# Performance work log

Measured on AMD Instinct MI355X. Metric: run time of the kernel, lower is better.

## Reference

```python
import jax, jax.numpy as jnp
import numpy as np

N_TRANSFORMS = 24
N_INIT = 5
SOFT_BLEND = 5.0
MAX_STEPS = 8   # reduced from 50 for reference runtime; same per-step math
CVG = 1e-5
DVG = 1.0
EPS = 1e-6


def posi_enc(x):
    # min_deg=0, max_deg=4, append_identity: [...,3] -> [...,27]
    scales = jnp.asarray([1.0, 2.0, 4.0, 8.0], x.dtype)
    xb = (x[..., None, :] * scales[:, None]).reshape(x.shape[:-1] + (12,))
    return jnp.concatenate([x, jnp.sin(xb), jnp.cos(xb)], axis=-1)


def mlp(h, params):
    for W, b in params[:-1]:
        h = jax.nn.relu(h @ W + b)
    W, b = params[-1]
    return h @ W + b


def setup_inputs() -> dict:
    key = jax.random.key(0)
    ks = jax.random.split(key, 16)
    B, N, J = 1, 32768, N_TRANSFORMS
    x = jax.random.normal(ks[0], (B, N, 3), jnp.float32)
    bone_pts = jax.random.normal(ks[1], (J, 3), jnp.float32)

    def near_id(k):
        A = jnp.eye(4, dtype=jnp.float32) + 0.05 * jax.random.normal(k, (J, 4, 4), jnp.float32)
        return A.at[:, 3, :].set(jnp.asarray([0.0, 0.0, 0.0, 1.0], jnp.float32))

    inp = dict(
        x=x, bone_pts=bone_pts,
        transforms=near_id(ks[2]), delta_transforms=near_id(ks[3]),
        W0=0.1 * jax.random.normal(ks[4], (27, 128), jnp.float32), b0=jnp.zeros((128,), jnp.float32),
        W1=0.1 * jax.random.normal(ks[5], (128, 128), jnp.float32), b1=jnp.zeros((128,), jnp.float32),
        W2=0.1 * jax.random.normal(ks[6], (128, 128), jnp.float32), b2=jnp.zeros((128,), jnp.float32),
        W3=0.1 * jax.random.normal(ks[7], (128, 128), jnp.float32), b3=jnp.zeros((128,), jnp.float32),
        W4=0.1 * jax.random.normal(ks[8], (128, 25), jnp.float32), b4=jnp.zeros((25,), jnp.float32),
    )
    return inp


def reference(x, bone_pts, transforms, delta_transforms, W0, b0, W1, b1, W2, b2, W3, b3, W4, b4):
    params = [(W0, b0), (W1, b1), (W2, b2), (W3, b3), (W4, b4)]
    B, N, _ = x.shape
    I = N_INIT + 1  # with_bkgd appends identity init
    dt = x.dtype

    # ---- _initialize_canonical: KNN over bone distances, gather delta transforms
    d = jnp.linalg.norm(x[:, :, None, :] - bone_pts, axis=-1)          # [B,N,J]
    idx = jax.lax.top_k(-d, N_INIT)[1]                                  # [B,N,5]
    Tsel = delta_transforms[idx]                                        # [B,N,5,4,4]
    eye4 = jnp.broadcast_to(jnp.eye(4, dtype=dt), (B, N, 1, 4, 4))
    Tinit = jnp.concatenate([Tsel, eye4], axis=2)                       # [B,N,I,4,4]
    xh = jnp.concatenate([x, jnp.ones_like(x[..., :1])], axis=-1)
    xc0 = jnp.einsum('bnipq,bnq->bnip', Tinit[..., :3, :4], xh)         # [B,N,I,3]

    M = B * N * I
    target = jnp.broadcast_to(x[:, :, None, :], (B, N, I, 3)).reshape(M, 3)
    x0 = xc0.reshape(M, 3)
    Tfull = jnp.concatenate([transforms, jnp.eye(4, dtype=dt)[None]], axis=0)  # [J+1,4,4]

    def g(xc):  # forward-skinning residual g(x_cano) = LBS(x_cano) - x_world
        w = jax.nn.softmax(SOFT_BLEND * mlp(posi_enc(xc), params), axis=-1)   # [M,25]
        tf = jnp.einsum('mj,jpq->mpq', w, Tfull)                               # [M,4,4]
        return jnp.einsum('mpq,mq->mp', tf[:, :3, :3], xc) + tf[:, :3, 3] - target

    # ---- Broyden with dense per-point masking (replaces torch boolean indexing)
    Jinv0 = jnp.broadcast_to(jnp.eye(3, dtype=dt), (M, 3, 3))
    gx0 = g(x0)
    upd0 = -(Jinv0 @ gx0[:, :, None])[:, :, 0]
    norm0 = jnp.linalg.norm(gx0, axis=-1)
    zeros3 = jnp.zeros((M, 3), dt)
    state = (x0, gx0, Jinv0, upd0, x0, norm0, zeros3, zeros3, jnp.ones((M,), bool))

    def body(_, s):
        xk, gx, Jinv, upd, xopt, nopt, dx, dgx, mask = s
        m3 = mask[:, None]
        dx = jnp.where(m3, upd, dx)
        xk = jnp.where(m3, xk + dx, xk)
        gnew = g(xk)
        dgx = jnp.where(m3, gnew - gx, dgx)
        gx = jnp.where(m3, gx + dgx, gx)
        gn = jnp.linalg.norm(gx, axis=-1)
        better = gn < nopt
        nopt = jnp.where(better, gn, nopt)
        xopt = jnp.where(better[:, None], xk, xopt)
        mask = (nopt > CVG) & (gn < DVG)
        vT = dx[:, None, :] @ Jinv                                      # [M,1,3]
        a = dx[:, :, None] - Jinv @ dgx[:, :, None]                      # [M,3,1]
        b = vT @ dgx[:, :, None]                                         # [M,1,1]
        b = b + jnp.where(b >= 0, EPS, -EPS)
        Jinv = jnp.where(mask[:, None, None], Jinv + (a / b) @ vT, Jinv)
        upd = jnp.where(m3, -(Jinv @ gx[:, :, None])[:, :, 0], upd)
        return (xk, gx, Jinv, upd, xopt, nopt, dx, dgx, mask)

    state = jax.lax.fori_loop(0, MAX_STEPS, body, state)
    xopt, nopt = state[4], state[5]
    xopt = jax.lax.stop_gradient(xopt)  # torch detaches the root solve
    valid = nopt < CVG

    # differentiable final forward skinning at the found canonical points
    w = jax.nn.softmax(SOFT_BLEND * mlp(posi_enc(xopt), params), axis=-1)
    tf = jnp.einsum('mj,jpq->mpq', w, Tfull)
    xw = jnp.einsum('mpq,mq->mp', tf[:, :3, :3], xopt) + tf[:, :3, 3]

    return (xw.reshape(B, N, I, 3), xopt.reshape(B, N, I, 3),
            nopt.reshape(B, N, I), valid.reshape(B, N, I))
```

## Files before the change

### kernel.cpp

```cpp
#include <hip/hip_runtime.h>
#include <math.h>
#include <stdint.h>

#define BLOCK 64
#define PPW 32
#define NTILES 56

typedef float v2f __attribute__((ext_vector_type(2)));

__device__ __forceinline__ v2f mkv2(float a, float b) {
    v2f r; r.x = a; r.y = b; return r;
}
__device__ __forceinline__ v2f pkfma(v2f a, v2f b, v2f c) {
#if __has_builtin(__builtin_elementwise_fma)
    return __builtin_elementwise_fma(a, b, c);
#else
    return mkv2(fmaf(a.x, b.x, c.x), fmaf(a.y, b.y, c.y));
#endif
}
__device__ __forceinline__ float f4el(const float4& v, int r) {
    return (r == 0) ? v.x : (r == 1) ? v.y : (r == 2) ? v.z : v.w;
}

#define VMWAIT() asm volatile("s_waitcnt vmcnt(0)" ::: "memory")

__device__ __forceinline__ void stage_tile(const float* __restrict__ Wt, int t,
                                           float* dst, int lane) {
    const float* src = Wt + t * 1024 + lane * 4;
    float* d0 = dst + lane * 4;
    __builtin_amdgcn_global_load_lds(
        (const __attribute__((address_space(1))) uint32_t*)src,
        (__attribute__((address_space(3))) uint32_t*)d0, 16, 0, 0);
    __builtin_amdgcn_global_load_lds(
        (const __attribute__((address_space(1))) uint32_t*)(src + 256),
        (__attribute__((address_space(3))) uint32_t*)(d0 + 256), 16, 0, 0);
    __builtin_amdgcn_global_load_lds(
        (const __attribute__((address_space(1))) uint32_t*)(src + 512),
        (__attribute__((address_space(3))) uint32_t*)(d0 + 512), 16, 0, 0);
    __builtin_amdgcn_global_load_lds(
        (const __attribute__((address_space(1))) uint32_t*)(src + 768),
        (__attribute__((address_space(3))) uint32_t*)(d0 + 768), 16, 0, 0);
}

__global__ void prep_kernel(const float* __restrict__ W0, const float* __restrict__ W1,
                            const float* __restrict__ W2, const float* __restrict__ W3,
                            const float* __restrict__ W4, const float* __restrict__ b4,
                            float* __restrict__ Wt, float* __restrict__ b4p) {
    const int d = blockIdx.x * blockDim.x + threadIdx.x;
    if (d < NTILES * 1024) {
        const int t = d >> 10, w = d & 1023;
        float v;
        if (t < 52) {
            const int r = w >> 7, rem = w & 127;
            const int half = rem >> 6, q = (rem >> 2) & 15, jl = rem & 3;
            const int col = q * 8 + half * 4 + jl;
            if (t < 4)       { const int k = t * 8 + r;        v = (k < 27) ? W0[k * 128 + col] : 0.f; }
            else if (t < 20) { const int k = (t - 4) * 8 + r;  v = W1[k * 128 + col]; }
            else if (t < 36) { const int k = (t - 20) * 8 + r; v = W2[k * 128 + col]; }
            else             { const int k = (t - 36) * 8 + r; v = W3[k * 128 + col]; }
        } else {
            const int r = w >> 5, c = w & 31;
            const int k = (t - 52) * 32 + r;
            v = (c < 25) ? W4[k * 25 + c] : 0.f;
        }
        Wt[d] = v;
    }
    if (d < 32) b4p[d] = (d < 25) ? b4[d] : 0.f;
}

__device__ __forceinline__ void batch2(const float* wt, int kt, int cg,
                                       const float* hgg, int kh,
                                       v2f* __restrict__ acc) {
    const float4 w00 = *(const float4*)(wt + kt * 128 + cg * 4);
    const float4 w01 = *(const float4*)(wt + kt * 128 + 64 + cg * 4);
    const float4 w10 = *(const float4*)(wt + (kt + 1) * 128 + cg * 4);
    const float4 w11 = *(const float4*)(wt + (kt + 1) * 128 + 64 + cg * 4);
    v2f h[8];
#pragma unroll
    for (int j = 0; j < 8; ++j) h[j] = *(const v2f*)(hgg + j * 132 + kh);
    const v2f a0 = mkv2(w00.x, w00.y), a1 = mkv2(w00.z, w00.w);
    const v2f a2 = mkv2(w01.x, w01.y), a3 = mkv2(w01.z, w01.w);
    const v2f b0v = mkv2(w10.x, w10.y), b1v = mkv2(w10.z, w10.w);
    const v2f b2v = mkv2(w11.x, w11.y), b3v = mkv2(w11.z, w11.w);
#pragma unroll
    for (int j = 0; j < 8; ++j) {
        v2f hh = mkv2(h[j].x, h[j].x);
        acc[j * 4 + 0] = pkfma(hh, a0, acc[j * 4 + 0]);
        acc[j * 4 + 1] = pkfma(hh, a1, acc[j * 4 + 1]);
        acc[j * 4 + 2] = pkfma(hh, a2, acc[j * 4 + 2]);
        acc[j * 4 + 3] = pkfma(hh, a3, acc[j * 4 + 3]);
        hh = mkv2(h[j].y, h[j].y);
        acc[j * 4 + 0] = pkfma(hh, b0v, acc[j * 4 + 0]);
        acc[j * 4 + 1] = pkfma(hh, b1v, acc[j * 4 + 1]);
        acc[j * 4 + 2] = pkfma(hh, b2v, acc[j * 4 + 2]);
        acc[j * 4 + 3] = pkfma(hh, b3v, acc[j * 4 + 3]);
    }
}

template <int NT>
__device__ __forceinline__ void main_layer(const float* __restrict__ Wt,
                                           const float* __restrict__ bL,
                                           float (*wb)[1024], int& cur, int& gt,
                                           const float* hgg, float* hwr,
                                           int cg, int lane) {
    v2f acc[32];
    {
        const float4 bb0 = *(const float4*)(bL + 8 * cg);
        const float4 bb1 = *(const float4*)(bL + 8 * cg + 4);
#pragma unroll
        for (int j = 0; j < 8; ++j) {
            acc[j * 4 + 0] = mkv2(bb0.x, bb0.y);
            acc[j * 4 + 1] = mkv2(bb0.z, bb0.w);
            acc[j * 4 + 2] = mkv2(bb1.x, bb1.y);
            acc[j * 4 + 3] = mkv2(bb1.z, bb1.w);
        }
    }
#pragma unroll 1
    for (int t = 0; t < NT; ++t) {
        VMWAIT();
        stage_tile(Wt, (gt == 55) ? 0 : (gt + 1), &wb[cur ^ 1][0], lane);
        const float* wt = &wb[cur][0];
#pragma unroll
        for (int b = 0; b < 4; ++b)
            batch2(wt, b * 2, cg, hgg, t * 8 + b * 2, acc);
        cur ^= 1;
        ++gt;
    }
#pragma unroll
    for (int j = 0; j < 8; ++j) {
        float4 o0, o1;
        o0.x = fmaxf(acc[j * 4 + 0].x, 0.f); o0.y = fmaxf(acc[j * 4 + 0].y, 0.f);
        o0.z = fmaxf(acc[j * 4 + 1].x, 0.f); o0.w = fmaxf(acc[j * 4 + 1].y, 0.f);
        o1.x = fmaxf(acc[j * 4 + 2].x, 0.f); o1.y = fmaxf(acc[j * 4 + 2].y, 0.f);
        o1.z = fmaxf(acc[j * 4 + 3].x, 0.f); o1.w = fmaxf(acc[j * 4 + 3].y, 0.f);
        *(float4*)(hwr + j * 132) = o0;
        *(float4*)(hwr + j * 132 + 4) = o1;
    }
}

__global__ __launch_bounds__(BLOCK)
__attribute__((amdgpu_num_vgpr(128))) void snarf_kernel(
    const float* __restrict__ xin, const float* __restrict__ bone_pts,
    const float* __restrict__ transforms, const float* __restrict__ delta_tf,
    const float* __restrict__ Wt, const float* __restrict__ b0,
    const float* __restrict__ b1, const float* __restrict__ b2,
    const float* __restrict__ b3, const float* __restrict__ b4p,
    float* __restrict__ out, int Npts) {
    __shared__ float hL[4248];
    __shared__ float stL[25 * PPW];
    __shared__ float wb[2][1024];
    const int lane = threadIdx.x;
    const int cg = lane >> 2;
    const int gg = lane & 3;
    const int p32 = lane & 31;
    const int du = lane >> 5;
    const int M = Npts * 6;
    const int m = blockIdx.x * PPW + p32;
    const int mc = (m < M) ? m : (M - 1);
    const int n = mc / 6;
    const int i = mc - n * 6;

    float* hq = hL + p32 * 132 + ((p32 >> 3) << 3);
    const float* hgg = hL + gg * 1064;
    float* hwr = hL + gg * 1064 + 8 * cg;
    volatile float* st = &stL[p32];
#define STS(idx) st[(idx) * PPW]

    stage_tile(Wt, 0, &wb[0][0], lane);
    int cur = 0;

    const float tx = xin[n * 3 + 0], ty = xin[n * 3 + 1], tz = xin[n * 3 + 2];

    float xk0, xk1, xk2;
    if (i < 5) {
        float dprev = -1.0f;
        int jprev = -1;
        for (int r = 0; r <= i; ++r) {
            float bd = 3.4028235e38f;
            int bj = 0;
            for (int j = 0; j < 24; ++j) {
                const float ax = tx - bone_pts[j * 3 + 0];
                const float ay = ty - bone_pts[j * 3 + 1];
                const float az = tz - bone_pts[j * 3 + 2];
                const float d = sqrtf(ax * ax + ay * ay + az * az);
                const bool taken = (d < dprev) || (d == dprev && j <= jprev);
                if (!taken && d < bd) { bd = d; bj = j; }
            }
            dprev = bd;
            jprev = bj;
        }
        const float* T = delta_tf + jprev * 16;
        xk0 = fmaf(T[0], tx, fmaf(T[1], ty, fmaf(T[2], tz, T[3])));
        xk1 = fmaf(T[4], tx, fmaf(T[5], ty, fmaf(T[6], tz, T[7])));
        xk2 = fmaf(T[8], tx, fmaf(T[9], ty, fmaf(T[10], tz, T[11])));
    } else {
        xk0 = tx; xk1 = ty; xk2 = tz;
    }

    float gx0 = 0.f, gx1 = 0.f, gx2 = 0.f;
    bool mask = (m < M);

    for (int step = -1; step < 8; ++step) {
        bool m3 = mask;
        if (step >= 0) {
            if (__ballot(mask) == 0ull) break;
            if (m3) {
                const float u0 = STS(9), u1 = STS(10), u2 = STS(11);
                STS(12) = u0; STS(13) = u1; STS(14) = u2;
                xk0 += u0; xk1 += u1; xk2 += u2;
            }
        }
        const float cx0 = xk0, cx1 = xk1, cx2 = xk2;

        {
            const float fa = du ? 4.f : 1.f;
            float sax, cax, say, cay, saz, caz;
            float sbx, cbx, sby, cby, sbz, cbz;
            sincosf(fa * cx0, &sax, &cax);
            sincosf(fa * cx1, &say, &cay);
            sincosf(fa * cx2, &saz, &caz);
            sincosf(2.f * fa * cx0, &sbx, &cbx);
            sincosf(2.f * fa * cx1, &sby, &cby);
            sincosf(2.f * fa * cx2, &sbz, &cbz);
            const int sa = 3 + du * 6;
            hq[sa + 0] = sax; hq[sa + 1] = say; hq[sa + 2] = saz;
            hq[sa + 3] = sbx; hq[sa + 4] = sby; hq[sa + 5] = sbz;
            hq[sa + 12] = cax; hq[sa + 13] = cay; hq[sa + 14] = caz;
            hq[sa + 15] = cbx; hq[sa + 16] = cby; hq[sa + 17] = cbz;
            if (du == 0) {
                hq[0] = cx0; hq[1] = cx1; hq[2] = cx2;
            } else {
                hq[27] = 0.f; hq[28] = 0.f; hq[29] = 0.f; hq[30] = 0.f; hq[31] = 0.f;
            }
        }

        __builtin_amdgcn_s_setprio(1);
        int gt = 0;
        main_layer<4>(Wt, b0, wb, cur, gt, hgg, hwr, cg, lane);
        main_layer<16>(Wt, b1, wb, cur, gt, hgg, hwr, cg, lane);
        main_layer<16>(Wt, b2, wb, cur, gt, hgg, hwr, cg, lane);
        main_layer<16>(Wt, b3, wb, cur, gt, hgg, hwr, cg, lane);

        {
            v2f la[8];
            {
                const float* bc = b4p + du * 16;
                const float4 bb0 = *(const float4*)(bc);
                const float4 bb1 = *(const float4*)(bc + 4);
                const float4 bb2 = *(const float4*)(bc + 8);
                const float4 bb3 = *(const float4*)(bc + 12);
                la[0] = mkv2(bb0.x, bb0.y); la[1] = mkv2(bb0.z, bb0.w);
                la[2] = mkv2(bb1.x, bb1.y); la[3] = mkv2(bb1.z, bb1.w);
                la[4] = mkv2(bb2.x, bb2.y); la[5] = mkv2(bb2.z, bb2.w);
                la[6] = mkv2(bb3.x, bb3.y); la[7] = mkv2(bb3.z, bb3.w);
            }
#pragma unroll 1
            for (int t = 0; t < 4; ++t) {
                VMWAIT();
                stage_tile(Wt, (t < 3) ? (53 + t) : 0, &wb[cur ^ 1][0], lane);
                const float* wt = &wb[cur][0];
#pragma unroll 2
                for (int kb = 0; kb < 8; ++kb) {
                    const float4 h4 = *(const float4*)(hq + t * 32 + kb * 4);
#pragma unroll
                    for (int r = 0; r < 4; ++r) {
                        const float* wr = wt + (kb * 4 + r) * 32 + du * 16;
                        const float4 w0 = *(const float4*)(wr);
                        const float4 w1 = *(const float4*)(wr + 4);
                        const float4 w2 = *(const float4*)(wr + 8);
                        const float4 w3 = *(const float4*)(wr + 12);
                        const float hv = f4el(h4, r);
                        const v2f hh = mkv2(hv, hv);
                        la[0] = pkfma(hh, mkv2(w0.x, w0.y), la[0]);
                        la[1] = pkfma(hh, mkv2(w0.z, w0.w), la[1]);
                        la[2] = pkfma(hh, mkv2(w1.x, w1.y), la[2]);
                        la[3] = pkfma(hh, mkv2(w1.z, w1.w), la[3]);
                        la[4] = pkfma(hh, mkv2(w2.x, w2.y), la[4]);
                        la[5] = pkfma(hh, mkv2(w2.z, w2.w), la[5]);
                        la[6] = pkfma(hh, mkv2(w3.x, w3.y), la[6]);
                        la[7] = pkfma(hh, mkv2(w3.z, w3.w), la[7]);
                    }
                }
                cur ^= 1;
            }
            __builtin_amdgcn_s_setprio(0);
            float4 o0, o1, o2, o3;
            o0.x = la[0].x; o0.y = la[0].y; o0.z = la[1].x; o0.w = la[1].y;
            o1.x = la[2].x; o1.y = la[2].y; o1.z = la[3].x; o1.w = la[3].y;
            o2.x = la[4].x; o2.y = la[4].y; o2.z = la[5].x; o2.w = la[5].y;
            o3.x = la[6].x; o3.y = la[6].y; o3.z = la[7].x; o3.w = la[7].y;
            *(float4*)(hq + du * 16 + 0) = o0;
            *(float4*)(hq + du * 16 + 4) = o1;
            *(float4*)(hq + du * 16 + 8) = o2;
            *(float4*)(hq + du * 16 + 12) = o3;
        }

        float l25[25];
        {
            const float4 r0 = *(const float4*)(hq + 0);
            const float4 r1 = *(const float4*)(hq + 4);
            const float4 r2 = *(const float4*)(hq + 8);
            const float4 r3 = *(const float4*)(hq + 12);
            const float4 r4 = *(const float4*)(hq + 16);
            const float4 r5 = *(const float4*)(hq + 20);
            l25[0] = r0.x; l25[1] = r0.y; l25[2] = r0.z; l25[3] = r0.w;
            l25[4] = r1.x; l25[5] = r1.y; l25[6] = r1.z; l25[7] = r1.w;
            l25[8] = r2.x; l25[9] = r2.y; l25[10] = r2.z; l25[11] = r2.w;
            l25[12] = r3.x; l25[13] = r3.y; l25[14] = r3.z; l25[15] = r3.w;
            l25[16] = r4.x; l25[17] = r4.y; l25[18] = r4.z; l25[19] = r4.w;
            l25[20] = r5.x; l25[21] = r5.y; l25[22] = r5.z; l25[23] = r5.w;
            l25[24] = hq[24];
        }

        float zm = -3.4028235e38f;
#pragma unroll
        for (int j = 0; j < 25; ++j) {
            l25[j] = 5.0f * l25[j];
            zm = fmaxf(zm, l25[j]);
        }
        float ssum = 0.f;
#pragma unroll
        for (int j = 0; j < 25; ++j) {
            l25[j] = expf(l25[j] - zm);
            ssum += l25[j];
        }
        const float inv = 1.0f / ssum;

        float tf[12];
#pragma unroll
        for (int r = 0; r < 12; ++r) tf[r] = 0.f;
#pragma unroll
        for (int j = 0; j < 24; ++j) {
            const float wj = l25[j] * inv;
            const float* T = transforms + j * 16;
#pragma unroll
            for (int r = 0; r < 12; ++r) tf[r] = fmaf(wj, T[r], tf[r]);
        }
        {
            const float wj = l25[24] * inv;
            tf[0] += wj; tf[5] += wj; tf[10] += wj;
        }
        const float r0 = fmaf(tf[0], cx0, fmaf(tf[1], cx1, fmaf(tf[2], cx2, tf[3])));
        const float r1 = fmaf(tf[4], cx0, fmaf(tf[5], cx1, fmaf(tf[6], cx2, tf[7])));
        const float r2 = fmaf(tf[8], cx0, fmaf(tf[9], cx1, fmaf(tf[10], cx2, tf[11])));

        const float g0 = r0 - tx, g1 = r1 - ty, g2 = r2 - tz;

        if (step == -1) {
            gx0 = g0; gx1 = g1; gx2 = g2;
            const float gn = sqrtf(g0 * g0 + g1 * g1 + g2 * g2);
            STS(21) = gn;
            STS(9) = -g0; STS(10) = -g1; STS(11) = -g2;
            STS(18) = xk0; STS(19) = xk1; STS(20) = xk2;
            STS(22) = r0; STS(23) = r1; STS(24) = r2;
            STS(12) = 0.f; STS(13) = 0.f; STS(14) = 0.f;
            STS(15) = 0.f; STS(16) = 0.f; STS(17) = 0.f;
            STS(0) = 1.f; STS(1) = 0.f; STS(2) = 0.f;
            STS(3) = 0.f; STS(4) = 1.f; STS(5) = 0.f;
            STS(6) = 0.f; STS(7) = 0.f; STS(8) = 1.f;
        } else {
            float J00 = STS(0), J01 = STS(1), J02 = STS(2);
            float J10 = STS(3), J11 = STS(4), J12 = STS(5);
            float J20 = STS(6), J21 = STS(7), J22 = STS(8);
            const float dx0 = STS(12), dx1 = STS(13), dx2 = STS(14);
            float dg0 = STS(15), dg1 = STS(16), dg2 = STS(17);
            float nopt = STS(21);
            if (m3) {
                dg0 = g0 - gx0; dg1 = g1 - gx1; dg2 = g2 - gx2;
                gx0 += dg0; gx1 += dg1; gx2 += dg2;
                STS(15) = dg0; STS(16) = dg1; STS(17) = dg2;
            }
            const float gn = sqrtf(gx0 * gx0 + gx1 * gx1 + gx2 * gx2);
            const bool better = gn < nopt;
            if (better) {
                nopt = gn;
                STS(21) = gn;
                STS(18) = xk0; STS(19) = xk1; STS(20) = xk2;
                STS(22) = r0; STS(23) = r1; STS(24) = r2;
            }
            mask = (nopt > 1e-5f) && (gn < 1.0f) && (m < M);

            const float v0 = dx0 * J00 + dx1 * J10 + dx2 * J20;
            const float v1 = dx0 * J01 + dx1 * J11 + dx2 * J21;
            const float v2 = dx0 * J02 + dx1 * J12 + dx2 * J22;
            const float Jd0 = J00 * dg0 + J01 * dg1 + J02 * dg2;
            const float Jd1 = J10 * dg0 + J11 * dg1 + J12 * dg2;
            const float Jd2 = J20 * dg0 + J21 * dg1 + J22 * dg2;
            const float a0 = dx0 - Jd0, a1 = dx1 - Jd1, a2 = dx2 - Jd2;
            float bden = v0 * dg0 + v1 * dg1 + v2 * dg2;
            bden += (bden >= 0.f) ? 1e-6f : -1e-6f;
            if (mask) {
                const float q0 = a0 / bden, q1 = a1 / bden, q2 = a2 / bden;
                J00 = fmaf(q0, v0, J00); J01 = fmaf(q0, v1, J01); J02 = fmaf(q0, v2, J02);
                J10 = fmaf(q1, v0, J10); J11 = fmaf(q1, v1, J11); J12 = fmaf(q1, v2, J12);
                J20 = fmaf(q2, v0, J20); J21 = fmaf(q2, v1, J21); J22 = fmaf(q2, v2, J22);
                STS(0) = J00; STS(1) = J01; STS(2) = J02;
                STS(3) = J10; STS(4) = J11; STS(5) = J12;
                STS(6) = J20; STS(7) = J21; STS(8) = J22;
            }
            if (m3) {
                STS(9) = -(J00 * gx0 + J01 * gx1 + J02 * gx2);
                STS(10) = -(J10 * gx0 + J11 * gx1 + J12 * gx2);
                STS(11) = -(J20 * gx0 + J21 * gx1 + J22 * gx2);
            }
        }
    }

    if (du == 0 && m < M) {
        const float nopt = STS(21);
        out[(size_t)m * 3 + 0] = STS(22);
        out[(size_t)m * 3 + 1] = STS(23);
        out[(size_t)m * 3 + 2] = STS(24);
        float* xopt_out = out + (size_t)M * 3;
        xopt_out[(size_t)m * 3 + 0] = STS(18);
        xopt_out[(size_t)m * 3 + 1] = STS(19);
        xopt_out[(size_t)m * 3 + 2] = STS(20);
        out[(size_t)M * 6 + m] = nopt;
        out[(size_t)M * 7 + m] = (nopt < 1e-5f) ? 1.0f : 0.0f;
    }
#undef STS
}

extern "C" void kernel_launch(void* const* d_in, const int* in_sizes, int n_in,
                              void* d_out, int out_size, void* d_ws, size_t ws_size,
                              hipStream_t stream) {
    const float* x = (const float*)d_in[0];
    const float* bone_pts = (const float*)d_in[1];
    const float* transforms = (const float*)d_in[2];
    const float* delta_tf = (const float*)d_in[3];
    const float* W0 = (const float*)d_in[4];
    const float* b0 = (const float*)d_in[5];
    const float* W1 = (const float*)d_in[6];
    const float* b1 = (const float*)d_in[7];
    const float* W2 = (const float*)d_in[8];
    const float* b2 = (const float*)d_in[9];
    const float* W3 = (const float*)d_in[10];
    const float* b3 = (const float*)d_in[11];
    const float* W4 = (const float*)d_in[12];
    const float* b4 = (const float*)d_in[13];
    float* out = (float*)d_out;

    float* Wt = (float*)d_ws;
    float* b4p = Wt + NTILES * 1024;

    prep_kernel<<<(NTILES * 1024 + 255) / 256, 256, 0, stream>>>(
        W0, W1, W2, W3, W4, b4, Wt, b4p);

    const int Npts = in_sizes[0] / 3;
    const int M = Npts * 6;
    const int blocks = (M + PPW - 1) / PPW;
    snarf_kernel<<<blocks, BLOCK, 0, stream>>>(
        x, bone_pts, transforms, delta_tf, Wt, b0, b1, b2, b3, b4p, out, Npts);
}
```

Before: 1.965 ms.

## Share staged MLP weight tiles across two waves with triple-buffered LDS

The block grows from one wave to two, and both waves share each weight tile staged into LDS. This halves the per-wave global-to-LDS traffic. The weight buffer becomes a three-slot ring with a prefetch distance of two, synchronised by partial vmcnt waits plus block barriers. Early exit now goes through per-wave flags in shared memory. A wave that has finished must still step through the tile pipeline without computing, so barrier coupling can make one wave wait on the other.

```diff
diff --git a/kernel.cpp b/kernel.cpp
--- a/kernel.cpp
+++ b/kernel.cpp
@@ -2,8 +2,8 @@
 #include <math.h>
 #include <stdint.h>
 
-#define BLOCK 64
-#define PPW 32
+#define BLOCK 128
+#define PPB 64
 #define NTILES 56
 
 typedef float v2f __attribute__((ext_vector_type(2)));
@@ -22,25 +22,24 @@
     return (r == 0) ? v.x : (r == 1) ? v.y : (r == 2) ? v.z : v.w;
 }
 
-#define VMWAIT() asm volatile("s_waitcnt vmcnt(0)" ::: "memory")
-
 __device__ __forceinline__ void stage_tile(const float* __restrict__ Wt, int t,
-                                           float* dst, int lane) {
-    const float* src = Wt + t * 1024 + lane * 4;
-    float* d0 = dst + lane * 4;
+                                           float* dst, int tid) {
+    const float* src = Wt + t * 1024 + tid * 4;
+    float* d0 = dst + tid * 4;
     __builtin_amdgcn_global_load_lds(
         (const __attribute__((address_space(1))) uint32_t*)src,
         (__attribute__((address_space(3))) uint32_t*)d0, 16, 0, 0);
     __builtin_amdgcn_global_load_lds(
-        (const __attribute__((address_space(1))) uint32_t*)(src + 256),
-        (__attribute__((address_space(3))) uint32_t*)(d0 + 256), 16, 0, 0);
-    __builtin_amdgcn_global_load_lds(
         (const __attribute__((address_space(1))) uint32_t*)(src + 512),
         (__attribute__((address_space(3))) uint32_t*)(d0 + 512), 16, 0, 0);
-    __builtin_amdgcn_global_load_lds(
-        (const __attribute__((address_space(1))) uint32_t*)(src + 768),
-        (__attribute__((address_space(3))) uint32_t*)(d0 + 768), 16, 0, 0);
-}
+}
+
+#define TILE_SYNC()                                          \
+    do {                                                     \
+        asm volatile("s_waitcnt vmcnt(2)" ::: "memory");     \
+        __builtin_amdgcn_s_barrier();                        \
+        __builtin_amdgcn_sched_barrier(0);                   \
+    } while (0)
 
 __global__ void prep_kernel(const float* __restrict__ W0, const float* __restrict__ W1,
                             const float* __restrict__ W2, const float* __restrict__ W3,
@@ -102,7 +101,7 @@
                                            const float* __restrict__ bL,
                                            float (*wb)[1024], int& cur, int& gt,
                                            const float* hgg, float* hwr,
-                                           int cg, int lane) {
+                                           int cg, int tid) {
     v2f acc[32];
     {
         const float4 bb0 = *(const float4*)(bL + 8 * cg);
@@ -117,13 +116,17 @@
     }
 #pragma unroll 1
     for (int t = 0; t < NT; ++t) {
-        VMWAIT();
-        stage_tile(Wt, (gt == 55) ? 0 : (gt + 1), &wb[cur ^ 1][0], lane);
+        TILE_SYNC();
+        {
+            const int nst = gt + 2;
+            const int c2 = (cur >= 1) ? (cur - 1) : 2;
+            stage_tile(Wt, (nst >= NTILES) ? (nst - NTILES) : nst, &wb[c2][0], tid);
+        }
         const float* wt = &wb[cur][0];
 #pragma unroll
         for (int b = 0; b < 4; ++b)
             batch2(wt, b * 2, cg, hgg, t * 8 + b * 2, acc);
-        cur ^= 1;
+        cur = (cur == 2) ? 0 : (cur + 1);
         ++gt;
     }
 #pragma unroll
@@ -146,27 +149,32 @@
     const float* __restrict__ b1, const float* __restrict__ b2,
     const float* __restrict__ b3, const float* __restrict__ b4p,
     float* __restrict__ out, int Npts) {
-    __shared__ float hL[4248];
-    __shared__ float stL[25 * PPW];
-    __shared__ float wb[2][1024];
-    const int lane = threadIdx.x;
+    __shared__ float hL[2][4248];
+    __shared__ float stL[25 * PPB];
+    __shared__ float wb[3][1024];
+    __shared__ int flags[2];
+    const int tid = threadIdx.x;
+    const int wid = tid >> 6;
+    const int lane = tid & 63;
     const int cg = lane >> 2;
     const int gg = lane & 3;
     const int p32 = lane & 31;
     const int du = lane >> 5;
     const int M = Npts * 6;
-    const int m = blockIdx.x * PPW + p32;
+    const int m = blockIdx.x * PPB + wid * 32 + p32;
     const int mc = (m < M) ? m : (M - 1);
     const int n = mc / 6;
     const int i = mc - n * 6;
 
-    float* hq = hL + p32 * 132 + ((p32 >> 3) << 3);
-    const float* hgg = hL + gg * 1064;
-    float* hwr = hL + gg * 1064 + 8 * cg;
-    volatile float* st = &stL[p32];
-#define STS(idx) st[(idx) * PPW]
-
-    stage_tile(Wt, 0, &wb[0][0], lane);
+    float* hWv = &hL[wid][0];
+    float* hq = hWv + p32 * 132 + ((p32 >> 3) << 3);
+    const float* hgg = hWv + gg * 1064;
+    float* hwr = hWv + gg * 1064 + 8 * cg;
+    volatile float* st = &stL[wid * 32 + p32];
+#define STS(idx) st[(idx) * PPB]
+
+    stage_tile(Wt, 0, &wb[0][0], tid);
+    stage_tile(Wt, 1, &wb[1][0], tid);
     int cur = 0;
 
     const float tx = xin[n * 3 + 0], ty = xin[n * 3 + 1], tz = xin[n * 3 + 2];
@@ -203,208 +211,235 @@
     for (int step = -1; step < 8; ++step) {
         bool m3 = mask;
         if (step >= 0) {
-            if (__ballot(mask) == 0ull) break;
+            __syncthreads();
+            if ((flags[0] | flags[1]) == 0) break;
             if (m3) {
                 const float u0 = STS(9), u1 = STS(10), u2 = STS(11);
                 STS(12) = u0; STS(13) = u1; STS(14) = u2;
                 xk0 += u0; xk1 += u1; xk2 += u2;
             }
         }
-        const float cx0 = xk0, cx1 = xk1, cx2 = xk2;
-
-        {
-            const float fa = du ? 4.f : 1.f;
-            float sax, cax, say, cay, saz, caz;
-            float sbx, cbx, sby, cby, sbz, cbz;
-            sincosf(fa * cx0, &sax, &cax);
-            sincosf(fa * cx1, &say, &cay);
-            sincosf(fa * cx2, &saz, &caz);
-            sincosf(2.f * fa * cx0, &sbx, &cbx);
-            sincosf(2.f * fa * cx1, &sby, &cby);
-            sincosf(2.f * fa * cx2, &sbz, &cbz);
-            const int sa = 3 + du * 6;
-            hq[sa + 0] = sax; hq[sa + 1] = say; hq[sa + 2] = saz;
-            hq[sa + 3] = sbx; hq[sa + 4] = sby; hq[sa + 5] = sbz;
-            hq[sa + 12] = cax; hq[sa + 13] = cay; hq[sa + 14] = caz;
-            hq[sa + 15] = cbx; hq[sa + 16] = cby; hq[sa + 17] = cbz;
-            if (du == 0) {
-                hq[0] = cx0; hq[1] = cx1; hq[2] = cx2;
-            } else {
-                hq[27] = 0.f; hq[28] = 0.f; hq[29] = 0.f; hq[30] = 0.f; hq[31] = 0.f;
-            }
-        }
-
-        __builtin_amdgcn_s_setprio(1);
-        int gt = 0;
-        main_layer<4>(Wt, b0, wb, cur, gt, hgg, hwr, cg, lane);
-        main_layer<16>(Wt, b1, wb, cur, gt, hgg, hwr, cg, lane);
-        main_layer<16>(Wt, b2, wb, cur, gt, hgg, hwr, cg, lane);
-        main_layer<16>(Wt, b3, wb, cur, gt, hgg, hwr, cg, lane);
-
-        {
-            v2f la[8];
+        const bool wskip = (__ballot(mask) == 0ull);
+
+        if (wskip) {
+            int gt = 0;
+#pragma unroll 1
+            for (int t = 0; t < NTILES; ++t) {
+                TILE_SYNC();
+                const int nst = gt + 2;
+                const int c2 = (cur >= 1) ? (cur - 1) : 2;
+                stage_tile(Wt, (nst >= NTILES) ? (nst - NTILES) : nst, &wb[c2][0], tid);
+                cur = (cur == 2) ? 0 : (cur + 1);
+                ++gt;
+            }
+        } else {
+            const float cx0 = xk0, cx1 = xk1, cx2 = xk2;
+
             {
-                const float* bc = b4p + du * 16;
-                const float4 bb0 = *(const float4*)(bc);
-                const float4 bb1 = *(const float4*)(bc + 4);
-                const float4 bb2 = *(const float4*)(bc + 8);
-                const float4 bb3 = *(const float4*)(bc + 12);
-                la[0] = mkv2(bb0.x, bb0.y); la[1] = mkv2(bb0.z, bb0.w);
-                la[2] = mkv2(bb1.x, bb1.y); la[3] = mkv2(bb1.z, bb1.w);
-                la[4] = mkv2(bb2.x, bb2.y); la[5] = mkv2(bb2.z, bb2.w);
-                la[6] = mkv2(bb3.x, bb3.y); la[7] = mkv2(bb3.z, bb3.w);
-            }
+                const float fa = du ? 4.f : 1.f;
+                float sax, cax, say, cay, saz, caz;
+                float sbx, cbx, sby, cby, sbz, cbz;
+                sincosf(fa * cx0, &sax, &cax);
+                sincosf(fa * cx1, &say, &cay);
+                sincosf(fa * cx2, &saz, &caz);
+                sincosf(2.f * fa * cx0, &sbx, &cbx);
+                sincosf(2.f * fa * cx1, &sby, &cby);
+                sincosf(2.f * fa * cx2, &sbz, &cbz);
+                const int sa = 3 + du * 6;
+                hq[sa + 0] = sax; hq[sa + 1] = say; hq[sa + 2] = saz;
+                hq[sa + 3] = sbx; hq[sa + 4] = sby; hq[sa + 5] = sbz;
+                hq[sa + 12] = cax; hq[sa + 13] = cay; hq[sa + 14] = caz;
+                hq[sa + 15] = cbx; hq[sa + 16] = cby; hq[sa + 17] = cbz;
+                if (du == 0) {
+                    hq[0] = cx0; hq[1] = cx1; hq[2] = cx2;
+                } else {
+                    hq[27] = 0.f; hq[28] = 0.f; hq[29] = 0.f; hq[30] = 0.f; hq[31] = 0.f;
+                }
+            }
+
+            __builtin_amdgcn_s_setprio(1);
+            int gt = 0;
+            main_layer<4>(Wt, b0, wb, cur, gt, hgg, hwr, cg, tid);
+            main_layer<16>(Wt, b1, wb, cur, gt, hgg, hwr, cg, tid);
+            main_layer<16>(Wt, b2, wb, cur, gt, hgg, hwr, cg, tid);
+            main_layer<16>(Wt, b3, wb, cur, gt, hgg, hwr, cg, tid);
+
+            {
+                v2f la[8];
+                {
+                    const float* bc = b4p + du * 16;
+                    const float4 bb0 = *(const float4*)(bc);
+                    const float4 bb1 = *(const float4*)(bc + 4);
+                    const float4 bb2 = *(const float4*)(bc + 8);
+                    const float4 bb3 = *(const float4*)(bc + 12);
+                    la[0] = mkv2(bb0.x, bb0.y); la[1] = mkv2(bb0.z, bb0.w);
+                    la[2] = mkv2(bb1.x, bb1.y); la[3] = mkv2(bb1.z, bb1.w);
+                    la[4] = mkv2(bb2.x, bb2.y); la[5] = mkv2(bb2.z, bb2.w);
+                    la[6] = mkv2(bb3.x, bb3.y); la[7] = mkv2(bb3.z, bb3.w);
+                }
 #pragma unroll 1
-            for (int t = 0; t < 4; ++t) {
-                VMWAIT();
-                stage_tile(Wt, (t < 3) ? (53 + t) : 0, &wb[cur ^ 1][0], lane);
-                const float* wt = &wb[cur][0];
+                for (int t = 0; t < 4; ++t) {
+                    TILE_SYNC();
+                    {
+                        const int nst = gt + 2;
+                        const int c2 = (cur >= 1) ? (cur - 1) : 2;
+                        stage_tile(Wt, (nst >= NTILES) ? (nst - NTILES) : nst, &wb[c2][0], tid);
+                    }
+                    const float* wt = &wb[cur][0];
 #pragma unroll 2
-                for (int kb = 0; kb < 8; ++kb) {
-                    const float4 h4 = *(const float4*)(hq + t * 32 + kb * 4);
-#pragma unroll
-                    for (int r = 0; r < 4; ++r) {
-                        const float* wr = wt + (kb * 4 + r) * 32 + du * 16;
-                        const float4 w0 = *(const float4*)(wr);
-                        const float4 w1 = *(const float4*)(wr + 4);
-                        const float4 w2 = *(const float4*)(wr + 8);
-                        const float4 w3 = *(const float4*)(wr + 12);
-                        const float hv = f4el(h4, r);
-                        const v2f hh = mkv2(hv, hv);
-                        la[0] = pkfma(hh, mkv2(w0.x, w0.y), la[0]);
-                        la[1] = pkfma(hh, mkv2(w0.z, w0.w), la[1]);
-                        la[2] = pkfma(hh, mkv2(w1.x, w1.y), la[2]);
-                        la[3] = pkfma(hh, mkv2(w1.z, w1.w), la[3]);
-                        la[4] = pkfma(hh, mkv2(w2.x, w2.y), la[4]);
-                        la[5] = pkfma(hh, mkv2(w2.z, w2.w), la[5]);
-                        la[6] = pkfma(hh, mkv2(w3.x, w3.y), la[6]);
-                        la[7] = pkfma(hh, mkv2(w3.z, w3.w), la[7]);
+                    for (int kb = 0; kb < 8; ++kb) {
+                        const float4 h4 = *(const float4*)(hq + t * 32 + kb * 4);
+#pragma unroll
+                        for (int r = 0; r < 4; ++r) {
+                            const float* wr = wt + (kb * 4 + r) * 32 + du * 16;
+                            const float4 w0 = *(const float4*)(wr);
+                            const float4 w1 = *(const float4*)(wr + 4);
+                            const float4 w2 = *(const float4*)(wr + 8);
+                            const float4 w3 = *(const float4*)(wr + 12);
+                            const float hv = f4el(h4, r);
+                            const v2f hh = mkv2(hv, hv);
+                            la[0] = pkfma(hh, mkv2(w0.x, w0.y), la[0]);
+                            la[1] = pkfma(hh, mkv2(w0.z, w0.w), la[1]);
+                            la[2] = pkfma(hh, mkv2(w1.x, w1.y), la[2]);
+                            la[3] = pkfma(hh, mkv2(w1.z, w1.w), la[3]);
+                            la[4] = pkfma(hh, mkv2(w2.x, w2.y), la[4]);
+                            la[5] = pkfma(hh, mkv2(w2.z, w2.w), la[5]);
+                            la[6] = pkfma(hh, mkv2(w3.x, w3.y), la[6]);
+                            la[7] = pkfma(hh, mkv2(w3.z, w3.w), la[7]);
+                        }
                     }
-                }
-                cur ^= 1;
-            }
-            __builtin_amdgcn_s_setprio(0);
-            float4 o0, o1, o2, o3;
-            o0.x = la[0].x; o0.y = la[0].y; o0.z = la[1].x; o0.w = la[1].y;
-            o1.x = la[2].x; o1.y = la[2].y; o1.z = la[3].x; o1.w = la[3].y;
-            o2.x = la[4].x; o2.y = la[4].y; o2.z = la[5].x; o2.w = la[5].y;
-            o3.x = la[6].x; o3.y = la[6].y; o3.z = la[7].x; o3.w = la[7].y;
-            *(float4*)(hq + du * 16 + 0) = o0;
-            *(float4*)(hq + du * 16 + 4) = o1;
-            *(float4*)(hq + du * 16 + 8) = o2;
-            *(float4*)(hq + du * 16 + 12) = o3;
-        }
-
-        float l25[25];
-        {
-            const float4 r0 = *(const float4*)(hq + 0);
-            const float4 r1 = *(const float4*)(hq + 4);
-            const float4 r2 = *(const float4*)(hq + 8);
-            const float4 r3 = *(const float4*)(hq + 12);
-            const float4 r4 = *(const float4*)(hq + 16);
-            const float4 r5 = *(const float4*)(hq + 20);
-            l25[0] = r0.x; l25[1] = r0.y; l25[2] = r0.z; l25[3] = r0.w;
-            l25[4] = r1.x; l25[5] = r1.y; l25[6] = r1.z; l25[7] = r1.w;
-            l25[8] = r2.x; l25[9] = r2.y; l25[10] = r2.z; l25[11] = r2.w;
-            l25[12] = r3.x; l25[13] = r3.y; l25[14] = r3.z; l25[15] = r3.w;
-            l25[16] = r4.x; l25[17] = r4.y; l25[18] = r4.z; l25[19] = r4.w;
-            l25[20] = r5.x; l25[21] = r5.y; l25[22] = r5.z; l25[23] = r5.w;
-            l25[24] = hq[24];
-        }
-
-        float zm = -3.4028235e38f;
-#pragma unroll
-        for (int j = 0; j < 25; ++j) {
-            l25[j] = 5.0f * l25[j];
-            zm = fmaxf(zm, l25[j]);
-        }
-        float ssum = 0.f;
-#pragma unroll
-        for (int j = 0; j < 25; ++j) {
-            l25[j] = expf(l25[j] - zm);
-            ssum += l25[j];
-        }
-        const float inv = 1.0f / ssum;
-
-        float tf[12];
-#pragma unroll
-        for (int r = 0; r < 12; ++r) tf[r] = 0.f;
-#pragma unroll
-        for (int j = 0; j < 24; ++j) {
-            const float wj = l25[j] * inv;
-            const float* T = transforms + j * 16;
-#pragma unroll
-            for (int r = 0; r < 12; ++r) tf[r] = fmaf(wj, T[r], tf[r]);
-        }
-        {
-            const float wj = l25[24] * inv;
-            tf[0] += wj; tf[5] += wj; tf[10] += wj;
-        }
-        const float r0 = fmaf(tf[0], cx0, fmaf(tf[1], cx1, fmaf(tf[2], cx2, tf[3])));
-        const float r1 = fmaf(tf[4], cx0, fmaf(tf[5], cx1, fmaf(tf[6], cx2, tf[7])));
-        const float r2 = fmaf(tf[8], cx0, fmaf(tf[9], cx1, fmaf(tf[10], cx2, tf[11])));
-
-        const float g0 = r0 - tx, g1 = r1 - ty, g2 = r2 - tz;
-
-        if (step == -1) {
-            gx0 = g0; gx1 = g1; gx2 = g2;
-            const float gn = sqrtf(g0 * g0 + g1 * g1 + g2 * g2);
-            STS(21) = gn;
-            STS(9) = -g0; STS(10) = -g1; STS(11) = -g2;
-            STS(18) = xk0; STS(19) = xk1; STS(20) = xk2;
-            STS(22) = r0; STS(23) = r1; STS(24) = r2;
-            STS(12) = 0.f; STS(13) = 0.f; STS(14) = 0.f;
-            STS(15) = 0.f; STS(16) = 0.f; STS(17) = 0.f;
-            STS(0) = 1.f; STS(1) = 0.f; STS(2) = 0.f;
-            STS(3) = 0.f; STS(4) = 1.f; STS(5) = 0.f;
-            STS(6) = 0.f; STS(7) = 0.f; STS(8) = 1.f;
-        } else {
-            float J00 = STS(0), J01 = STS(1), J02 = STS(2);
-            float J10 = STS(3), J11 = STS(4), J12 = STS(5);
-            float J20 = STS(6), J21 = STS(7), J22 = STS(8);
-            const float dx0 = STS(12), dx1 = STS(13), dx2 = STS(14);
-            float dg0 = STS(15), dg1 = STS(16), dg2 = STS(17);
-            float nopt = STS(21);
-            if (m3) {
-                dg0 = g0 - gx0; dg1 = g1 - gx1; dg2 = g2 - gx2;
-                gx0 += dg0; gx1 += dg1; gx2 += dg2;
-                STS(15) = dg0; STS(16) = dg1; STS(17) = dg2;
-            }
-            const float gn = sqrtf(gx0 * gx0 + gx1 * gx1 + gx2 * gx2);
-            const bool better = gn < nopt;
-            if (better) {
-                nopt = gn;
+                    cur = (cur == 2) ? 0 : (cur + 1);
+                    ++gt;
+                }
+                __builtin_amdgcn_s_setprio(0);
+                float4 o0, o1, o2, o3;
+                o0.x = la[0].x; o0.y = la[0].y; o0.z = la[1].x; o0.w = la[1].y;
+                o1.x = la[2].x; o1.y = la[2].y; o1.z = la[3].x; o1.w = la[3].y;
+                o2.x = la[4].x; o2.y = la[4].y; o2.z = la[5].x; o2.w = la[5].y;
+                o3.x = la[6].x; o3.y = la[6].y; o3.z = la[7].x; o3.w = la[7].y;
+                *(float4*)(hq + du * 16 + 0) = o0;
+                *(float4*)(hq + du * 16 + 4) = o1;
+                *(float4*)(hq + du * 16 + 8) = o2;
+                *(float4*)(hq + du * 16 + 12) = o3;
+            }
+
+            float l25[25];
+            {
+                const float4 r0 = *(const float4*)(hq + 0);
+                const float4 r1 = *(const float4*)(hq + 4);
+                const float4 r2 = *(const float4*)(hq + 8);
+                const float4 r3 = *(const float4*)(hq + 12);
+                const float4 r4 = *(const float4*)(hq + 16);
+                const float4 r5 = *(const float4*)(hq + 20);
+                l25[0] = r0.x; l25[1] = r0.y; l25[2] = r0.z; l25[3] = r0.w;
+                l25[4] = r1.x; l25[5] = r1.y; l25[6] = r1.z; l25[7] = r1.w;
+                l25[8] = r2.x; l25[9] = r2.y; l25[10] = r2.z; l25[11] = r2.w;
+                l25[12] = r3.x; l25[13] = r3.y; l25[14] = r3.z; l25[15] = r3.w;
+                l25[16] = r4.x; l25[17] = r4.y; l25[18] = r4.z; l25[19] = r4.w;
+                l25[20] = r5.x; l25[21] = r5.y; l25[22] = r5.z; l25[23] = r5.w;
+                l25[24] = hq[24];
+            }
+
+            float zm = -3.4028235e38f;
+#pragma unroll
+            for (int j = 0; j < 25; ++j) {
+                l25[j] = 5.0f * l25[j];
+                zm = fmaxf(zm, l25[j]);
+            }
+            float ssum = 0.f;
+#pragma unroll
+            for (int j = 0; j < 25; ++j) {
+                l25[j] = expf(l25[j] - zm);
+                ssum += l25[j];
+            }
+            const float inv = 1.0f / ssum;
+
+            float tf[12];
+#pragma unroll
+            for (int r = 0; r < 12; ++r) tf[r] = 0.f;
+#pragma unroll
+            for (int j = 0; j < 24; ++j) {
+                const float wj = l25[j] * inv;
+                const float* T = transforms + j * 16;
+#pragma unroll
+                for (int r = 0; r < 12; ++r) tf[r] = fmaf(wj, T[r], tf[r]);
+            }
+            {
+                const float wj = l25[24] * inv;
+                tf[0] += wj; tf[5] += wj; tf[10] += wj;
+            }
+            const float r0 = fmaf(tf[0], cx0, fmaf(tf[1], cx1, fmaf(tf[2], cx2, tf[3])));
+            const float r1 = fmaf(tf[4], cx0, fmaf(tf[5], cx1, fmaf(tf[6], cx2, tf[7])));
+            const float r2 = fmaf(tf[8], cx0, fmaf(tf[9], cx1, fmaf(tf[10], cx2, tf[11])));
+
+            const float g0 = r0 - tx, g1 = r1 - ty, g2 = r2 - tz;
+
+            if (step == -1) {
+                gx0 = g0; gx1 = g1; gx2 = g2;
+                const float gn = sqrtf(g0 * g0 + g1 * g1 + g2 * g2);
                 STS(21) = gn;
+                STS(9) = -g0; STS(10) = -g1; STS(11) = -g2;
                 STS(18) = xk0; STS(19) = xk1; STS(20) = xk2;
                 STS(22) = r0; STS(23) = r1; STS(24) = r2;
-            }
-            mask = (nopt > 1e-5f) && (gn < 1.0f) && (m < M);
-
-            const float v0 = dx0 * J00 + dx1 * J10 + dx2 * J20;
-            const float v1 = dx0 * J01 + dx1 * J11 + dx2 * J21;
-            const float v2 = dx0 * J02 + dx1 * J12 + dx2 * J22;
-            const float Jd0 = J00 * dg0 + J01 * dg1 + J02 * dg2;
-            const float Jd1 = J10 * dg0 + J11 * dg1 + J12 * dg2;
-            const float Jd2 = J20 * dg0 + J21 * dg1 + J22 * dg2;
-            const float a0 = dx0 - Jd0, a1 = dx1 - Jd1, a2 = dx2 - Jd2;
-            float bden = v0 * dg0 + v1 * dg1 + v2 * dg2;
-            bden += (bden >= 0.f) ? 1e-6f : -1e-6f;
-            if (mask) {
-                const float q0 = a0 / bden, q1 = a1 / bden, q2 = a2 / bden;
-                J00 = fmaf(q0, v0, J00); J01 = fmaf(q0, v1, J01); J02 = fmaf(q0, v2, J02);
-                J10 = fmaf(q1, v0, J10); J11 = fmaf(q1, v1, J11); J12 = fmaf(q1, v2, J12);
-                J20 = fmaf(q2, v0, J20); J21 = fmaf(q2, v1, J21); J22 = fmaf(q2, v2, J22);
-                STS(0) = J00; STS(1) = J01; STS(2) = J02;
-                STS(3) = J10; STS(4) = J11; STS(5) = J12;
-                STS(6) = J20; STS(7) = J21; STS(8) = J22;
-            }
-            if (m3) {
-                STS(9) = -(J00 * gx0 + J01 * gx1 + J02 * gx2);
-                STS(10) = -(J10 * gx0 + J11 * gx1 + J12 * gx2);
-                STS(11) = -(J20 * gx0 + J21 * gx1 + J22 * gx2);
-            }
-        }
-    }
+                STS(12) = 0.f; STS(13) = 0.f; STS(14) = 0.f;
+                STS(15) = 0.f; STS(16) = 0.f; STS(17) = 0.f;
+                STS(0) = 1.f; STS(1) = 0.f; STS(2) = 0.f;
+                STS(3) = 0.f; STS(4) = 1.f; STS(5) = 0.f;
+                STS(6) = 0.f; STS(7) = 0.f; STS(8) = 1.f;
+            } else {
+                float J00 = STS(0), J01 = STS(1), J02 = STS(2);
+                float J10 = STS(3), J11 = STS(4), J12 = STS(5);
+                float J20 = STS(6), J21 = STS(7), J22 = STS(8);
+                const float dx0 = STS(12), dx1 = STS(13), dx2 = STS(14);
+                float dg0 = STS(15), dg1 = STS(16), dg2 = STS(17);
+                float nopt = STS(21);
+                if (m3) {
+                    dg0 = g0 - gx0; dg1 = g1 - gx1; dg2 = g2 - gx2;
+                    gx0 += dg0; gx1 += dg1; gx2 += dg2;
+                    STS(15) = dg0; STS(16) = dg1; STS(17) = dg2;
+                }
+                const float gn = sqrtf(gx0 * gx0 + gx1 * gx1 + gx2 * gx2);
+                const bool better = gn < nopt;
+                if (better) {
+                    nopt = gn;
+                    STS(21) = gn;
+                    STS(18) = xk0; STS(19) = xk1; STS(20) = xk2;
+                    STS(22) = r0; STS(23) = r1; STS(24) = r2;
+                }
+                mask = (nopt > 1e-5f) && (gn < 1.0f) && (m < M);
+
+                const float v0 = dx0 * J00 + dx1 * J10 + dx2 * J20;
+                const float v1 = dx0 * J01 + dx1 * J11 + dx2 * J21;
+                const float v2 = dx0 * J02 + dx1 * J12 + dx2 * J22;
+                const float Jd0 = J00 * dg0 + J01 * dg1 + J02 * dg2;
+                const float Jd1 = J10 * dg0 + J11 * dg1 + J12 * dg2;
+                const float Jd2 = J20 * dg0 + J21 * dg1 + J22 * dg2;
+                const float a0 = dx0 - Jd0, a1 = dx1 - Jd1, a2 = dx2 - Jd2;
+                float bden = v0 * dg0 + v1 * dg1 + v2 * dg2;
+                bden += (bden >= 0.f) ? 1e-6f : -1e-6f;
+                if (mask) {
+                    const float q0 = a0 / bden, q1 = a1 / bden, q2 = a2 / bden;
+                    J00 = fmaf(q0, v0, J00); J01 = fmaf(q0, v1, J01); J02 = fmaf(q0, v2, J02);
+                    J10 = fmaf(q1, v0, J10); J11 = fmaf(q1, v1, J11); J12 = fmaf(q1, v2, J12);
+                    J20 = fmaf(q2, v0, J20); J21 = fmaf(q2, v1, J21); J22 = fmaf(q2, v2, J22);
+                    STS(0) = J00; STS(1) = J01; STS(2) = J02;
+                    STS(3) = J10; STS(4) = J11; STS(5) = J12;
+                    STS(6) = J20; STS(7) = J21; STS(8) = J22;
+                }
+                if (m3) {
+                    STS(9) = -(J00 * gx0 + J01 * gx1 + J02 * gx2);
+                    STS(10) = -(J10 * gx0 + J11 * gx1 + J12 * gx2);
+                    STS(11) = -(J20 * gx0 + J21 * gx1 + J22 * gx2);
+                }
+            }
+        }
+        {
+            const unsigned long long b = __ballot(mask);
+            if (lane == 0) flags[wid] = (b != 0ull) ? 1 : 0;
+        }
+    }
+
+    asm volatile("s_waitcnt vmcnt(0)" ::: "memory");
 
     if (du == 0 && m < M) {
         const float nopt = STS(21);
@@ -448,7 +483,7 @@
 
     const int Npts = in_sizes[0] / 3;
     const int M = Npts * 6;
-    const int blocks = (M + PPW - 1) / PPW;
+    const int blocks = (M + PPB - 1) / PPB;
     snarf_kernel<<<blocks, BLOCK, 0, stream>>>(
         x, bone_pts, transforms, delta_tf, Wt, b0, b1, b2, b3, b4p, out, Npts);
 }
```

New measurement: 1.948 ms. Within noise of the previous version (-0.9%).
